# Performance work log

Measured on AMD Instinct MI355X. Metric: run time of the kernel, lower is better.

Reference implementation:

```python
import jax, jax.numpy as jnp
import numpy as np

DN = ('NCDHW', 'OIDHW', 'NCDHW')

def conv3d(x, w, b):
    # kernel 3, padding 1, stride 1 -> SAME
    y = jax.lax.conv_general_dilated(x, w, window_strides=(1, 1, 1), padding='SAME', dimension_numbers=DN)
    return y + b[None, :, None, None, None]

def setup_inputs() -> dict:
    key = jax.random.key(0)
    ks = jax.random.split(key, 7)
    C, Cqk = 64, 8  # in_channels, in_channels // 8
    x = jax.random.normal(ks[0], (2, C, 20, 20, 20), dtype=jnp.float32)
    fan_qk = C * 27
    fan_v = C * 27
    wq = jax.random.normal(ks[1], (Cqk, C, 3, 3, 3), dtype=jnp.float32) / np.sqrt(fan_qk)
    bq = jax.random.normal(ks[2], (Cqk,), dtype=jnp.float32) * 0.01
    wk = jax.random.normal(ks[3], (Cqk, C, 3, 3, 3), dtype=jnp.float32) / np.sqrt(fan_qk)
    bk = jax.random.normal(ks[4], (Cqk,), dtype=jnp.float32) * 0.01
    wv = jax.random.normal(ks[5], (C, C, 3, 3, 3), dtype=jnp.float32) / np.sqrt(fan_v)
    bv = jax.random.normal(ks[6], (C,), dtype=jnp.float32) * 0.01
    return {'x': x, 'wq': wq, 'bq': bq, 'wk': wk, 'bk': bk, 'wv': wv, 'bv': bv}

def reference(x, wq, bq, wk, bk, wv, bv):
    b, C, h, w, d = x.shape
    n = h * w * d
    M = conv3d(x, wq, bq).reshape(b, -1, n)   # (b, C/8, n)
    N = conv3d(x, wk, bk).reshape(b, -1, n)   # (b, C/8, n)
    V = conv3d(x, wv, bv).reshape(b, C, n)    # (b, C, n)
    # B[b,i,j] = softmax_j( sum_c M[b,c,i] * N[b,c,j] )  (no scale factor, as in source)
    scores = jnp.einsum('bci,bcj->bij', M, N)
    B = jax.nn.softmax(scores, axis=-1)
    # GSA[b,c,i] = sum_j V[b,c,j] * B[b,i,j]
    out = jnp.einsum('bcj,bij->bci', V, B).reshape(b, C, h, w, d)
    return out
```

## Files before the change

kernel.cpp:

```cpp
#include <hip/hip_runtime.h>
#include <hip/hip_bf16.h>
#include <math.h>

#define NSP 8000
#define CIN 64
#define LOG2E 1.4426950408889634f

typedef __attribute__((ext_vector_type(8)))  short    bf16x8;
typedef __attribute__((ext_vector_type(4)))  float    f32x4;
typedef __attribute__((ext_vector_type(16))) float    f32x16;
typedef __attribute__((ext_vector_type(8)))  _Float16 f16x8;
typedef __attribute__((ext_vector_type(2)))  __fp16   fp16x2;

__device__ __forceinline__ ushort f2bf(float f) {
    unsigned u = __float_as_uint(f);
    unsigned r = (u + 0x7fffu + ((u >> 16) & 1u)) >> 16;
    return (ushort)r;
}

__global__ __launch_bounds__(64) void prep_kernel(
    const float* __restrict__ wq, const float* __restrict__ wk,
    const float* __restrict__ wv, const float* __restrict__ x,
    ushort* __restrict__ wtap, ushort* __restrict__ xpad)
{
    const int bid = blockIdx.x;
    if (bid < 2160) {
        const int tap = bid / 80;
        const int co  = bid % 80;
        const int ci  = threadIdx.x;
        float v;
        if (co < 8)       v = wq[(co * 64 + ci) * 27 + tap];
        else if (co < 16) v = wk[((co - 8) * 64 + ci) * 27 + tap];
        else              v = wv[((co - 16) * 64 + ci) * 27 + tap];
        wtap[((size_t)tap * 80 + co) * 64 + ci] = f2bf(v);
    } else {
        const int bx  = bid - 2160;
        const int b   = bx / 484;
        const int rem = bx % 484;
        const int zp  = rem / 22, yp = rem % 22;
        const int ci  = threadIdx.x;
        const bool zy = (zp >= 1 && zp <= 20) && (yp >= 1 && yp <= 20);
        const float* xb = x + ((size_t)b * 64 + ci) * NSP + (zp - 1) * 400 + (yp - 1) * 20;
        ushort* op = xpad + (size_t)b * 681472 + (size_t)(zp * 484 + yp * 22) * 64 + ci;
        #pragma unroll
        for (int xp = 0; xp < 22; ++xp) {
            float v = 0.0f;
            if (zy && xp >= 1 && xp <= 20) v = xb[xp - 1];
            op[xp * 64] = f2bf(v);
        }
    }
}

__global__ __launch_bounds__(512, 2) void conv_mfma_kernel(
    const ushort* __restrict__ xpad, const ushort* __restrict__ wtap,
    const float* __restrict__ bq, const float* __restrict__ bk,
    const float* __restrict__ bv,
    _Float16* __restrict__ Qt, _Float16* __restrict__ Kt, _Float16* __restrict__ VT)
{
    const int t  = threadIdx.x;
    const int l  = t & 63;
    const int w  = t >> 6;
    const int sp = w >> 2;
    const int st = w & 3;
    const int bx = blockIdx.x * 4 + st;
    const int b  = blockIdx.y;
    const int s  = bx * 16 + (l & 15);
    const int z  = s / 400;
    const int r0 = s % 400;
    const int y  = r0 / 20;
    const int xx = r0 % 20;
    const int kq = (l >> 4) * 8;

    const ushort* xb = xpad + (size_t)b * 681472
                     + (size_t)(z * 484 + y * 22 + xx) * 64 + kq;
    const ushort* wl = wtap + (l & 15) * 64 + kq;

    f32x4 acc[5];
    #pragma unroll
    for (int ct = 0; ct < 5; ++ct) acc[ct] = (f32x4)0.0f;

    const int tap0 = sp ? 14 : 0;
    const int tap1 = sp ? 27 : 14;

    for (int tap = tap0; tap < tap1; ++tap) {
        const int dz = tap / 9;
        const int r9 = tap % 9;
        const int dy = r9 / 3;
        const int dx = r9 % 3;
        const ushort* xp2 = xb + (size_t)(dz * 484 + dy * 22 + dx) * 64;
        const bf16x8 b0 = *(const bf16x8*)(xp2);
        const bf16x8 b1 = *(const bf16x8*)(xp2 + 32);
        const ushort* wp = wl + (size_t)tap * 80 * 64;
        #pragma unroll
        for (int ct = 0; ct < 5; ++ct) {
            const bf16x8 a0 = *(const bf16x8*)(wp + ct * 16 * 64);
            const bf16x8 a1 = *(const bf16x8*)(wp + ct * 16 * 64 + 32);
            acc[ct] = __builtin_amdgcn_mfma_f32_16x16x32_bf16(a0, b0, acc[ct], 0, 0, 0);
            acc[ct] = __builtin_amdgcn_mfma_f32_16x16x32_bf16(a1, b1, acc[ct], 0, 0, 0);
        }
    }

    __shared__ float lacc[4][64][20];
    if (sp == 1) {
        #pragma unroll
        for (int ct = 0; ct < 5; ++ct)
            *(f32x4*)&lacc[st][l][ct * 4] = acc[ct];
    }
    __syncthreads();
    if (sp == 0) {
        #pragma unroll
        for (int ct = 0; ct < 5; ++ct) {
            #pragma unroll
            for (int r = 0; r < 4; ++r) {
                const float v = acc[ct][r] + lacc[st][l][ct * 4 + r];
                const int co = ct * 16 + (l >> 4) * 4 + r;
                if (co < 8)
                    Qt[((size_t)b * NSP + s) * 8 + co] = (_Float16)((v + bq[co]) * LOG2E);
                else if (co < 16)
                    Kt[((size_t)b * NSP + s) * 8 + (co - 8)] = (_Float16)(v + bk[co - 8]);
                else {
                    const int c = co - 16;
                    VT[(size_t)b * 512000 + ((size_t)bx * 64 + c) * 16 + (l & 15)] =
                        (_Float16)(v + bv[c]);
                }
            }
        }
    }
}

__global__ __launch_bounds__(512, 4) void attn_kernel(
    const _Float16* __restrict__ Qt, const _Float16* __restrict__ Kt,
    const _Float16* __restrict__ VT, float* __restrict__ out)
{
    const int t  = threadIdx.x;
    const int l  = t & 63;
    const int w  = t >> 6;
    const int b  = blockIdx.y;
    const int i0 = blockIdx.x * 32;
    const int il = l & 31;
    const int hi = l >> 5;

    const _Float16* Qtb = Qt + (size_t)b * NSP * 8;
    const _Float16* Ktb = Kt + (size_t)b * NSP * 8;
    const _Float16* VTb = VT + (size_t)b * 512000;

    __shared__ __align__(16) char smem[34816];
    _Float16* p_base = (_Float16*)smem;
    float*    mrg    = (float*)smem;
    float*    mml    = (float*)(smem + 32768);
    float*    lsm    = (float*)(smem + 33792);

    _Float16* pw = p_base + w * 1152;

    f16x8 qf = (f16x8)(_Float16)0.0f;
    if (l < 32) qf = *(const f16x8*)&Qtb[(size_t)(i0 + il) * 8];

    float m = -INFINITY, lsum = 0.0f;
    f32x16 acc0 = (f32x16)0.0f, acc1 = (f32x16)0.0f;
    const f32x16 zero16 = (f32x16)0.0f;

#define LOADK(JT, KF) { KF = (f16x8)(_Float16)0.0f;                         \
        if (l < 32) KF = *(const f16x8*)&Ktb[(size_t)((JT) * 32 + il) * 8]; }
#define LOADV(JT, VF) { const int jb = (JT) * 2;                            \
        VF##00 = *(const f16x8*)&VTb[((size_t)(jb + 0) * 64 + il) * 16 + 8 * hi];      \
        VF##01 = *(const f16x8*)&VTb[((size_t)(jb + 1) * 64 + il) * 16 + 8 * hi];      \
        VF##10 = *(const f16x8*)&VTb[((size_t)(jb + 0) * 64 + 32 + il) * 16 + 8 * hi]; \
        VF##11 = *(const f16x8*)&VTb[((size_t)(jb + 1) * 64 + 32 + il) * 16 + 8 * hi]; }

    int jt = w;
    f16x8 kf, vf00, vf01, vf10, vf11;
    LOADK(jt, kf);
    LOADV(jt, vf);

    while (jt < 250) {
        const int jn = jt + 8;
        const bool has = (jn < 250);
        f16x8 kf_n, vn00, vn01, vn10, vn11;
        if (has) { LOADK(jn, kf_n); LOADV(jn, vn); }

        f32x16 sacc = __builtin_amdgcn_mfma_f32_32x32x16_f16(kf, qf, zero16, 0, 0, 0);

        float pm = sacc[0];
        #pragma unroll
        for (int r = 1; r < 16; ++r) pm = fmaxf(pm, sacc[r]);
        pm = fmaxf(pm, __shfl_xor(pm, 32));

        if (__any(pm > m + 8.0f)) {
            const float mn = fmaxf(m, pm);
            const float sc = __builtin_amdgcn_exp2f(m - mn);
            #pragma unroll
            for (int r = 0; r < 16; ++r) { acc0[r] *= sc; acc1[r] *= sc; }
            lsum *= sc;
            m = mn;
        }

        float ps = 0.0f;
        #pragma unroll
        for (int r = 0; r < 16; ++r) {
            const float p = __builtin_amdgcn_exp2f(sacc[r] - m);
            sacc[r] = p;
            ps += p;
        }
        ps += __shfl_xor(ps, 32);
        lsum += ps;

        #pragma unroll
        for (int g = 0; g < 4; ++g) {
            union { fp16x2 h[2]; uint2 u; } pk;
            pk.h[0] = __builtin_amdgcn_cvt_pkrtz(sacc[g * 4 + 0], sacc[g * 4 + 1]);
            pk.h[1] = __builtin_amdgcn_cvt_pkrtz(sacc[g * 4 + 2], sacc[g * 4 + 3]);
            *(uint2*)(pw + il * 36 + g * 8 + hi * 4) = pk.u;
        }
        asm volatile("s_waitcnt lgkmcnt(0)" ::: "memory");
        __builtin_amdgcn_sched_barrier(0);

        __builtin_amdgcn_s_setprio(1);
        {
            const f16x8 pf0 = *(const f16x8*)(pw + il * 36 + 8 * hi);
            acc0 = __builtin_amdgcn_mfma_f32_32x32x16_f16(vf00, pf0, acc0, 0, 0, 0);
            acc1 = __builtin_amdgcn_mfma_f32_32x32x16_f16(vf10, pf0, acc1, 0, 0, 0);
            const f16x8 pf1 = *(const f16x8*)(pw + il * 36 + 16 + 8 * hi);
            acc0 = __builtin_amdgcn_mfma_f32_32x32x16_f16(vf01, pf1, acc0, 0, 0, 0);
            acc1 = __builtin_amdgcn_mfma_f32_32x32x16_f16(vf11, pf1, acc1, 0, 0, 0);
        }
        __builtin_amdgcn_s_setprio(0);

        if (has) {
            kf = kf_n;
            vf00 = vn00; vf01 = vn01; vf10 = vn10; vf11 = vn11;
        }
        jt = jn;
    }
#undef LOADK
#undef LOADV

    __syncthreads();
    if (l < 32) mml[w * 32 + il] = m;
    __syncthreads();
    float gm = mml[il];
    #pragma unroll
    for (int ww = 1; ww < 8; ++ww) gm = fmaxf(gm, mml[ww * 32 + il]);
    const float f = __builtin_amdgcn_exp2f(m - gm);
    if (l < 32) lsm[w * 32 + il] = lsum * f;
    #pragma unroll
    for (int r = 0; r < 16; ++r) { acc0[r] *= f; acc1[r] *= f; }

    float* ob = out + (size_t)b * 64 * NSP + i0;

    #pragma unroll
    for (int r = 0; r < 16; ++r) {
        const int cl = (r & 3) + 8 * (r >> 2) + 4 * hi;
        mrg[w * 1024 + cl * 32 + il] = acc0[r];
    }
    __syncthreads();
    #pragma unroll
    for (int rep = 0; rep < 2; ++rep) {
        const int e = t + rep * 512;
        const int c = e >> 5, i = e & 31;
        float sv = 0.0f, lg = 0.0f;
        #pragma unroll
        for (int ww = 0; ww < 8; ++ww) {
            sv += mrg[ww * 1024 + c * 32 + i];
            lg += lsm[ww * 32 + i];
        }
        float inv;
        asm("v_rcp_f32 %0, %1" : "=v"(inv) : "v"(lg));
        ob[(size_t)c * NSP + i] = sv * inv;
    }
    __syncthreads();

    #pragma unroll
    for (int r = 0; r < 16; ++r) {
        const int cl = (r & 3) + 8 * (r >> 2) + 4 * hi;
        mrg[w * 1024 + cl * 32 + il] = acc1[r];
    }
    __syncthreads();
    #pragma unroll
    for (int rep = 0; rep < 2; ++rep) {
        const int e = t + rep * 512;
        const int c = e >> 5, i = e & 31;
        float sv = 0.0f, lg = 0.0f;
        #pragma unroll
        for (int ww = 0; ww < 8; ++ww) {
            sv += mrg[ww * 1024 + c * 32 + i];
            lg += lsm[ww * 32 + i];
        }
        float inv;
        asm("v_rcp_f32 %0, %1" : "=v"(inv) : "v"(lg));
        ob[(size_t)(32 + c) * NSP + i] = sv * inv;
    }
}

extern "C" void kernel_launch(void* const* d_in, const int* in_sizes, int n_in,
                              void* d_out, int out_size, void* d_ws, size_t ws_size,
                              hipStream_t stream) {
    const float* x  = (const float*)d_in[0];
    const float* wq = (const float*)d_in[1];
    const float* bq = (const float*)d_in[2];
    const float* wk = (const float*)d_in[3];
    const float* bk = (const float*)d_in[4];
    const float* wv = (const float*)d_in[5];
    const float* bv = (const float*)d_in[6];
    float* out = (float*)d_out;

    ushort*   wtap = (ushort*)d_ws;
    ushort*   xpad = (ushort*)((char*)d_ws + 278528);
    _Float16* Qt   = (_Float16*)((char*)d_ws + 3004416);
    _Float16* Kt   = (_Float16*)((char*)d_ws + 3260416);
    _Float16* VT   = (_Float16*)((char*)d_ws + 3516416);

    prep_kernel<<<dim3(3128), 64, 0, stream>>>(wq, wk, wv, x, wtap, xpad);
    conv_mfma_kernel<<<dim3(125, 2), 512, 0, stream>>>(xpad, wtap, bq, bk, bv, Qt, Kt, VT);
    attn_kernel<<<dim3(250, 2), 512, 0, stream>>>(Qt, Kt, VT, out);
}
```

Baseline: 158.7 us.

## Split conv taps 4-way, pass P via permlane swap instead of LDS

The conv kernel now splits the 27 taps across four wave groups per spatial tile instead of two, processes two tiles per block, and doubles the grid. Partial sums are reduced through a larger shared buffer. This gives more parallelism and shorter per-wave loops. In the attention kernel, the probability tile no longer round-trips through LDS; it is repacked in registers with v_permlane32_swap, and the max and sum reductions become trees. The cross-half sum shuffle is deferred to the end, and the attention launch bound changes from 4 to 2 blocks per CU. The changes aim to cut LDS traffic, waitcnt stalls and serial dependency chains, at the cost of extra shared-memory reduction work in the conv kernel and possible occupancy changes.

```diff
diff --git a/kernel.cpp b/kernel.cpp
--- a/kernel.cpp
+++ b/kernel.cpp
@@ -60,9 +60,9 @@
     const int t  = threadIdx.x;
     const int l  = t & 63;
     const int w  = t >> 6;
-    const int sp = w >> 2;
-    const int st = w & 3;
-    const int bx = blockIdx.x * 4 + st;
+    const int st = w & 1;
+    const int sp = w >> 1;
+    const int bx = blockIdx.x * 2 + st;
     const int b  = blockIdx.y;
     const int s  = bx * 16 + (l & 15);
     const int z  = s / 400;
@@ -79,8 +79,8 @@
     #pragma unroll
     for (int ct = 0; ct < 5; ++ct) acc[ct] = (f32x4)0.0f;
 
-    const int tap0 = sp ? 14 : 0;
-    const int tap1 = sp ? 27 : 14;
+    const int tap0 = sp * 7;
+    const int tap1 = (sp == 3) ? 27 : (tap0 + 7);
 
     for (int tap = tap0; tap < tap1; ++tap) {
         const int dz = tap / 9;
@@ -100,11 +100,11 @@
         }
     }
 
-    __shared__ float lacc[4][64][20];
-    if (sp == 1) {
+    __shared__ float lacc[3][2][64][20];
+    if (sp > 0) {
         #pragma unroll
         for (int ct = 0; ct < 5; ++ct)
-            *(f32x4*)&lacc[st][l][ct * 4] = acc[ct];
+            *(f32x4*)&lacc[sp - 1][st][l][ct * 4] = acc[ct];
     }
     __syncthreads();
     if (sp == 0) {
@@ -112,7 +112,8 @@
         for (int ct = 0; ct < 5; ++ct) {
             #pragma unroll
             for (int r = 0; r < 4; ++r) {
-                const float v = acc[ct][r] + lacc[st][l][ct * 4 + r];
+                const float v = acc[ct][r] + lacc[0][st][l][ct * 4 + r]
+                             + lacc[1][st][l][ct * 4 + r] + lacc[2][st][l][ct * 4 + r];
                 const int co = ct * 16 + (l >> 4) * 4 + r;
                 if (co < 8)
                     Qt[((size_t)b * NSP + s) * 8 + co] = (_Float16)((v + bq[co]) * LOG2E);
@@ -128,7 +129,7 @@
     }
 }
 
-__global__ __launch_bounds__(512, 4) void attn_kernel(
+__global__ __launch_bounds__(512, 2) void attn_kernel(
     const _Float16* __restrict__ Qt, const _Float16* __restrict__ Kt,
     const _Float16* __restrict__ VT, float* __restrict__ out)
 {
@@ -145,12 +146,9 @@
     const _Float16* VTb = VT + (size_t)b * 512000;
 
     __shared__ __align__(16) char smem[34816];
-    _Float16* p_base = (_Float16*)smem;
-    float*    mrg    = (float*)smem;
-    float*    mml    = (float*)(smem + 32768);
-    float*    lsm    = (float*)(smem + 33792);
-
-    _Float16* pw = p_base + w * 1152;
+    float* mrg = (float*)smem;
+    float* mml = (float*)(smem + 32768);
+    float* lsm = (float*)(smem + 33792);
 
     f16x8 qf = (f16x8)(_Float16)0.0f;
     if (l < 32) qf = *(const f16x8*)&Qtb[(size_t)(i0 + il) * 8];
@@ -180,12 +178,15 @@
 
         f32x16 sacc = __builtin_amdgcn_mfma_f32_32x32x16_f16(kf, qf, zero16, 0, 0, 0);
 
-        float pm = sacc[0];
-        #pragma unroll
-        for (int r = 1; r < 16; ++r) pm = fmaxf(pm, sacc[r]);
-        pm = fmaxf(pm, __shfl_xor(pm, 32));
+        float x0 = fmaxf(sacc[0], sacc[1]),   x1 = fmaxf(sacc[2], sacc[3]);
+        float x2 = fmaxf(sacc[4], sacc[5]),   x3 = fmaxf(sacc[6], sacc[7]);
+        float x4 = fmaxf(sacc[8], sacc[9]),   x5 = fmaxf(sacc[10], sacc[11]);
+        float x6 = fmaxf(sacc[12], sacc[13]), x7 = fmaxf(sacc[14], sacc[15]);
+        float pm = fmaxf(fmaxf(fmaxf(x0, x1), fmaxf(x2, x3)),
+                         fmaxf(fmaxf(x4, x5), fmaxf(x6, x7)));
 
         if (__any(pm > m + 8.0f)) {
+            pm = fmaxf(pm, __shfl_xor(pm, 32));
             const float mn = fmaxf(m, pm);
             const float sc = __builtin_amdgcn_exp2f(m - mn);
             #pragma unroll
@@ -194,35 +195,44 @@
             m = mn;
         }
 
-        float ps = 0.0f;
-        #pragma unroll
-        for (int r = 0; r < 16; ++r) {
-            const float p = __builtin_amdgcn_exp2f(sacc[r] - m);
-            sacc[r] = p;
-            ps += p;
-        }
-        ps += __shfl_xor(ps, 32);
-        lsum += ps;
-
-        #pragma unroll
-        for (int g = 0; g < 4; ++g) {
-            union { fp16x2 h[2]; uint2 u; } pk;
-            pk.h[0] = __builtin_amdgcn_cvt_pkrtz(sacc[g * 4 + 0], sacc[g * 4 + 1]);
-            pk.h[1] = __builtin_amdgcn_cvt_pkrtz(sacc[g * 4 + 2], sacc[g * 4 + 3]);
-            *(uint2*)(pw + il * 36 + g * 8 + hi * 4) = pk.u;
-        }
-        asm volatile("s_waitcnt lgkmcnt(0)" ::: "memory");
-        __builtin_amdgcn_sched_barrier(0);
+        #pragma unroll
+        for (int r = 0; r < 16; ++r)
+            sacc[r] = __builtin_amdgcn_exp2f(sacc[r] - m);
+        {
+            float s0 = (sacc[0] + sacc[1]) + (sacc[2] + sacc[3]);
+            float s1 = (sacc[4] + sacc[5]) + (sacc[6] + sacc[7]);
+            float s2 = (sacc[8] + sacc[9]) + (sacc[10] + sacc[11]);
+            float s3 = (sacc[12] + sacc[13]) + (sacc[14] + sacc[15]);
+            lsum += (s0 + s1) + (s2 + s3);
+        }
+
+        unsigned w0, w1, w2, w3, w4, w5, w6, w7;
+        {
+            union { fp16x2 h; unsigned u; } c;
+            c.h = __builtin_amdgcn_cvt_pkrtz(sacc[0],  sacc[1]);  w0 = c.u;
+            c.h = __builtin_amdgcn_cvt_pkrtz(sacc[2],  sacc[3]);  w1 = c.u;
+            c.h = __builtin_amdgcn_cvt_pkrtz(sacc[4],  sacc[5]);  w2 = c.u;
+            c.h = __builtin_amdgcn_cvt_pkrtz(sacc[6],  sacc[7]);  w3 = c.u;
+            c.h = __builtin_amdgcn_cvt_pkrtz(sacc[8],  sacc[9]);  w4 = c.u;
+            c.h = __builtin_amdgcn_cvt_pkrtz(sacc[10], sacc[11]); w5 = c.u;
+            c.h = __builtin_amdgcn_cvt_pkrtz(sacc[12], sacc[13]); w6 = c.u;
+            c.h = __builtin_amdgcn_cvt_pkrtz(sacc[14], sacc[15]); w7 = c.u;
+        }
+        unsigned A0 = w0, A2 = w2, A1 = w1, A3 = w3;
+        unsigned B0 = w4, B2 = w6, B1 = w5, B3 = w7;
+        asm("v_permlane32_swap_b32 %0, %1" : "+v"(A0), "+v"(A2));
+        asm("v_permlane32_swap_b32 %0, %1" : "+v"(A1), "+v"(A3));
+        asm("v_permlane32_swap_b32 %0, %1" : "+v"(B0), "+v"(B2));
+        asm("v_permlane32_swap_b32 %0, %1" : "+v"(B1), "+v"(B3));
+        union { unsigned u[4]; f16x8 v; } pf0u, pf1u;
+        pf0u.u[0] = A0; pf0u.u[1] = A1; pf0u.u[2] = A2; pf0u.u[3] = A3;
+        pf1u.u[0] = B0; pf1u.u[1] = B1; pf1u.u[2] = B2; pf1u.u[3] = B3;
 
         __builtin_amdgcn_s_setprio(1);
-        {
-            const f16x8 pf0 = *(const f16x8*)(pw + il * 36 + 8 * hi);
-            acc0 = __builtin_amdgcn_mfma_f32_32x32x16_f16(vf00, pf0, acc0, 0, 0, 0);
-            acc1 = __builtin_amdgcn_mfma_f32_32x32x16_f16(vf10, pf0, acc1, 0, 0, 0);
-            const f16x8 pf1 = *(const f16x8*)(pw + il * 36 + 16 + 8 * hi);
-            acc0 = __builtin_amdgcn_mfma_f32_32x32x16_f16(vf01, pf1, acc0, 0, 0, 0);
-            acc1 = __builtin_amdgcn_mfma_f32_32x32x16_f16(vf11, pf1, acc1, 0, 0, 0);
-        }
+        acc0 = __builtin_amdgcn_mfma_f32_32x32x16_f16(vf00, pf0u.v, acc0, 0, 0, 0);
+        acc1 = __builtin_amdgcn_mfma_f32_32x32x16_f16(vf10, pf0u.v, acc1, 0, 0, 0);
+        acc0 = __builtin_amdgcn_mfma_f32_32x32x16_f16(vf01, pf1u.v, acc0, 0, 0, 0);
+        acc1 = __builtin_amdgcn_mfma_f32_32x32x16_f16(vf11, pf1u.v, acc1, 0, 0, 0);
         __builtin_amdgcn_s_setprio(0);
 
         if (has) {
@@ -234,7 +244,7 @@
 #undef LOADK
 #undef LOADV
 
-    __syncthreads();
+    lsum += __shfl_xor(lsum, 32);
     if (l < 32) mml[w * 32 + il] = m;
     __syncthreads();
     float gm = mml[il];
@@ -310,6 +320,6 @@
     _Float16* VT   = (_Float16*)((char*)d_ws + 3516416);
 
     prep_kernel<<<dim3(3128), 64, 0, stream>>>(wq, wk, wv, x, wtap, xpad);
-    conv_mfma_kernel<<<dim3(125, 2), 512, 0, stream>>>(xpad, wtap, bq, bk, bv, Qt, Kt, VT);
+    conv_mfma_kernel<<<dim3(250, 2), 512, 0, stream>>>(xpad, wtap, bq, bk, bv, Qt, Kt, VT);
     attn_kernel<<<dim3(250, 2), 512, 0, stream>>>(Qt, Kt, VT, out);
 }
```

Result: faster. 152.6 us (-3.9%).
